# Optimization experiments

Measured on AMD Instinct MI355X. Metric: run time of the kernel, lower is better.

## Reference

```python
import jax, jax.numpy as jnp
import numpy as np

STRIDE = 1
PAD = 1
EXTENT = 3  # kernel footprint (ceil of max tap offset), 3x3 tap grid


def setup_inputs() -> dict:
    key = jax.random.key(0)
    k1, k2 = jax.random.split(key)
    B, Cin, H, W = 8, 64, 128, 128
    Cout, K = 64, 9
    x = jax.random.normal(k1, (B, Cin, H, W), dtype=jnp.float32)
    # per-tap weights, one scalar weight per (out_ch, in_ch, tap) -- op formula is 'x * w'
    weights = jax.random.normal(k2, (Cout, Cin, K), dtype=jnp.float32) * 0.05
    # 3x3 integer grid shifted by +0.4 -> non-integer offsets => bilinear (sub-pixel) gather
    base = jnp.stack(jnp.meshgrid(jnp.arange(3.0), jnp.arange(3.0), indexing='ij'), -1).reshape(9, 2)
    tap_offsets = (base + 0.4).astype(jnp.float32)  # [K, 2] (dy, dx)
    return {"x": x, "weights": weights, "tap_offsets": tap_offsets}


def _bilinear_tap(xp, dy, dx, H_out, W_out):
    # Gather xp at (oy*stride + dy, ox*stride + dx) with separable bilinear interp.
    Hp, Wp = xp.shape[-2], xp.shape[-1]
    y = jnp.arange(H_out, dtype=xp.dtype) * STRIDE + dy
    xc = jnp.arange(W_out, dtype=xp.dtype) * STRIDE + dx
    y0 = jnp.floor(y)
    x0 = jnp.floor(xc)
    fy = (y - y0)[None, None, :, None]
    fx = (xc - x0)[None, None, None, :]
    y0i = jnp.clip(y0.astype(jnp.int32), 0, Hp - 1)
    y1i = jnp.clip(y0.astype(jnp.int32) + 1, 0, Hp - 1)
    x0i = jnp.clip(x0.astype(jnp.int32), 0, Wp - 1)
    x1i = jnp.clip(x0.astype(jnp.int32) + 1, 0, Wp - 1)
    # interp rows first: [B, C, H_out, Wp]
    ry = xp[:, :, y0i, :] * (1.0 - fy) + xp[:, :, y1i, :] * fy
    # then columns: [B, C, H_out, W_out]
    return ry[:, :, :, x0i] * (1.0 - fx) + ry[:, :, :, x1i] * fx


def reference(x, weights, tap_offsets):
    B, Cin, H, W = x.shape
    K = weights.shape[-1]
    xp = jnp.pad(x, ((0, 0), (0, 0), (PAD, PAD), (PAD, PAD)))
    H_out = (H + 2 * PAD - EXTENT) // STRIDE + 1
    W_out = (W + 2 * PAD - EXTENT) // STRIDE + 1
    # gather all taps (loop over small fixed K=9, each fully vectorized over B,C,H,W)
    taps = [_bilinear_tap(xp, tap_offsets[k, 0], tap_offsets[k, 1], H_out, W_out)
            for k in range(K)]
    g = jnp.stack(taps, 0)  # [K, B, Cin, H_out, W_out]
    # per-tap op 'x * w', accumulated over taps and input channels
    return jnp.einsum('kbiyx,oik->boyx', g, weights)  # [B, Cout, H_out, W_out]
```

## Files before the change

### kernel.cpp

```cpp
#include <hip/hip_runtime.h>


#define CIN   64
#define COUT  64
#define HH    128
#define WW    128

typedef __attribute__((ext_vector_type(8)))  short bf16x8;
typedef __attribute__((ext_vector_type(4)))  float f32x4;
typedef __attribute__((ext_vector_type(16))) float f32x16;
typedef __attribute__((ext_vector_type(4)))  unsigned int u32x4;

__device__ __forceinline__ unsigned short f2bf(float f) {
  unsigned int u = __float_as_uint(f);
  u = (u + 0x7fffu + ((u >> 16) & 1u)) >> 16;
  return (unsigned short)u;
}

__global__ void make_wb(const float* __restrict__ wgt,
                        const float* __restrict__ off,
                        unsigned short* __restrict__ wb)
{
  int id = blockIdx.x * 64 + threadIdx.x;
  int o = id >> 6, c = id & 63;
  float W16[16];
  #pragma unroll
  for (int i = 0; i < 16; ++i) W16[i] = 0.f;
  for (int k = 0; k < 9; ++k) {
    float dy = off[2*k], dx = off[2*k+1];
    float fyf = floorf(dy), fxf = floorf(dx);
    int   iy = (int)fyf,   ix = (int)fxf;
    float fy = dy - fyf,   fx = dx - fxf;
    float wk = wgt[(o*CIN + c)*9 + k];
    W16[(iy  )*4 + ix  ] += wk * (1.f-fy)*(1.f-fx);
    W16[(iy  )*4 + ix+1] += wk * (1.f-fy)*fx;
    W16[(iy+1)*4 + ix  ] += wk * fy*(1.f-fx);
    W16[(iy+1)*4 + ix+1] += wk * fy*fx;
  }
  int g = c >> 4, half = (c >> 3) & 1, j = c & 7;
  int ni = o >> 5, l31 = o & 31;
  int lane = half*32 + l31;
  for (int tap = 0; tap < 16; ++tap) {
    int h8 = tap >> 3, rs8 = tap & 7;
    wb[(size_t)((((g*2 + h8)*16) + rs8*2 + ni)*64 + lane)*8 + j] = f2bf(W16[tap]);
  }
}

__global__ __launch_bounds__(128)
void transpose_x(const float* __restrict__ x, unsigned short* __restrict__ xt)
{
  const int bid = blockIdx.x;
  const int b   = bid / 131;
  const int yp  = bid - b * 131;
  const int t   = threadIdx.x;

  unsigned short* rowbase = xt + (size_t)(b*132 + yp)*8*132*8;

  if (yp == 0 || yp >= 129) {
    for (int i = t; i < 8*132; i += 128)
      *(u32x4*)&rowbase[i*8] = (u32x4){0u,0u,0u,0u};
    return;
  }
  const int gy = yp - 1;
  const int px = t;
  #pragma unroll
  for (int cq = 0; cq < 8; ++cq) {
    const float* ps = x + ((size_t)(b*CIN + cq*8)*HH + gy)*WW + px;
    float v[8];
    #pragma unroll
    for (int cc = 0; cc < 8; ++cc) v[cc] = ps[(size_t)cc*HH*WW];
    unsigned int pk[4];
    #pragma unroll
    for (int i = 0; i < 4; ++i)
      pk[i] = (unsigned int)f2bf(v[2*i]) | ((unsigned int)f2bf(v[2*i+1]) << 16);
    *(u32x4*)&rowbase[(cq*132 + px + 1)*8] = *(u32x4*)pk;
  }
  if (t < 32) {
    int cq = t >> 2, csel = t & 3;
    int col = (csel == 0) ? 0 : (128 + csel);
    *(u32x4*)&rowbase[(cq*132 + col)*8] = (u32x4){0u,0u,0u,0u};
  }
}

__global__ __launch_bounds__(256, 2)
void conv_mfma(const unsigned short* __restrict__ xt,
               const unsigned short* __restrict__ wb,
               float* __restrict__ out)
{
  const int wg = blockIdx.x;
  const int b  = wg & 7;
  const int i6 = wg >> 3;
  const int y0 = (i6 >> 1) * 4;
  const int x0 = (i6 & 1) * 64;
  const int t  = threadIdx.x;
  const int lane = t & 63;
  const int wave = t >> 6;
  const int l31  = lane & 31;
  const int half = lane >> 5;
  const int y    = y0 + wave;

  f32x16 acc[2][2];
  #pragma unroll
  for (int mi = 0; mi < 2; ++mi)
    #pragma unroll
    for (int ni = 0; ni < 2; ++ni)
      acc[mi][ni] = (f32x16)(0.f);

  const unsigned short* wl = wb + lane*8;

  const unsigned short* xbase = xt + (size_t)(b*132 + y)*8*132*8
                                   + (size_t)(x0 + l31)*8 + (size_t)half*132*8;

  bf16x8 aq[2][2], bq[2][2];

  auto loadB = [&](int g, int tap, bf16x8 (&dst)[2]) {
    int h8 = tap >> 3, rs8 = tap & 7;
    #pragma unroll
    for (int ni = 0; ni < 2; ++ni)
      dst[ni] = *(const bf16x8*)(wl + (size_t)(((g*2 + h8)*16) + rs8*2 + ni)*512);
  };
  auto loadA = [&](int g, int tap, bf16x8 (&dst)[2]) {
    int r = tap >> 2, s = tap & 3;
    const unsigned short* p = xbase + (size_t)(r*8*132 + g*2*132 + s)*8;
    #pragma unroll
    for (int mi = 0; mi < 2; ++mi)
      dst[mi] = *(const bf16x8*)(p + mi*32*8);
  };

  loadA(0, 0, aq[0]);
  loadB(0, 0, bq[0]);

  #pragma unroll
  for (int g = 0; g < 4; ++g) {
    #pragma unroll
    for (int tap = 0; tap < 16; ++tap) {
      if (tap < 15) {
        loadA(g, tap + 1, aq[(tap + 1) & 1]);
        loadB(g, tap + 1, bq[(tap + 1) & 1]);
      } else if (g < 3) {
        loadA(g + 1, 0, aq[0]);
        loadB(g + 1, 0, bq[0]);
      }
      const int sl = tap & 1;
      #pragma unroll
      for (int mi = 0; mi < 2; ++mi) {
        acc[mi][0] = __builtin_amdgcn_mfma_f32_32x32x16_bf16(aq[sl][mi], bq[sl][0], acc[mi][0], 0, 0, 0);
        acc[mi][1] = __builtin_amdgcn_mfma_f32_32x32x16_bf16(aq[sl][mi], bq[sl][1], acc[mi][1], 0, 0, 0);
      }
    }
  }

  #pragma unroll
  for (int mi = 0; mi < 2; ++mi) {
    #pragma unroll
    for (int ni = 0; ni < 2; ++ni) {
      int o = ni*32 + l31;
      float* dst = out + (((size_t)(b*COUT + o))*HH + y)*WW + x0 + mi*32 + 4*half;
      #pragma unroll
      for (int rg = 0; rg < 4; ++rg) {
        f32x4 v = (f32x4){acc[mi][ni][4*rg+0], acc[mi][ni][4*rg+1],
                          acc[mi][ni][4*rg+2], acc[mi][ni][4*rg+3]};
        *(f32x4*)(dst + 8*rg) = v;
      }
    }
  }
}

extern "C" void kernel_launch(void* const* d_in, const int* in_sizes, int n_in,
                              void* d_out, int out_size, void* d_ws, size_t ws_size,
                              hipStream_t stream)
{
  const float* x   = (const float*)d_in[0];
  const float* wgt = (const float*)d_in[1];
  const float* off = (const float*)d_in[2];
  float* out = (float*)d_out;

  unsigned short* wb = (unsigned short*)d_ws;
  unsigned short* xt = (unsigned short*)d_ws + 65536;

  make_wb<<<64, 64, 0, stream>>>(wgt, off, wb);
  transpose_x<<<8*131, 128, 0, stream>>>(x, xt);
  conv_mfma<<<512, 256, 0, stream>>>(xt, wb, out);
}
```

Baseline: 125.3 us.

## Stage input tile in LDS via global_load_lds and vectorize transpose

The conv kernel now copies a 7-row by 67-column input tile for all 64 channels into shared memory with direct global-to-LDS loads, then reads the A fragments from LDS. Previously each wave fetched overlapping tap windows from global memory, so neighbouring rows and shifted columns were loaded many times; staging the tile once removes that redundant global/L2 traffic. The weight fragments are now triple-buffered. The transpose kernel switches to 256 threads with float4 loads and a row pitch padded to 136, and its grid grows to cover 132 padded rows. The cost is about 64 KB of LDS per block, which limits occupancy to two blocks per CU, plus a block-wide barrier before any compute can start.

```diff
diff --git a/kernel.cpp b/kernel.cpp
--- a/kernel.cpp
+++ b/kernel.cpp
@@ -10,6 +10,9 @@
 typedef __attribute__((ext_vector_type(4)))  float f32x4;
 typedef __attribute__((ext_vector_type(16))) float f32x16;
 typedef __attribute__((ext_vector_type(4)))  unsigned int u32x4;
+
+#define AS1C(p) ((const __attribute__((address_space(1))) unsigned int*)(p))
+#define AS3P(p) ((__attribute__((address_space(3))) unsigned int*)(p))
 
 __device__ __forceinline__ unsigned short f2bf(float f) {
   unsigned int u = __float_as_uint(f);
@@ -46,47 +49,52 @@
   }
 }
 
-__global__ __launch_bounds__(128)
+__global__ __launch_bounds__(256)
 void transpose_x(const float* __restrict__ x, unsigned short* __restrict__ xt)
 {
   const int bid = blockIdx.x;
-  const int b   = bid / 131;
-  const int yp  = bid - b * 131;
+  const int b   = bid & 7;
+  const int yp  = bid >> 3;
   const int t   = threadIdx.x;
 
-  unsigned short* rowbase = xt + (size_t)(b*132 + yp)*8*132*8;
+  unsigned short* rowb = xt + (size_t)((b*132 + yp)*8)*136*8;
 
   if (yp == 0 || yp >= 129) {
-    for (int i = t; i < 8*132; i += 128)
-      *(u32x4*)&rowbase[i*8] = (u32x4){0u,0u,0u,0u};
+    for (int i = t; i < 8*136; i += 256)
+      *(u32x4*)&rowb[(size_t)i*8] = (u32x4){0u,0u,0u,0u};
     return;
   }
-  const int gy = yp - 1;
-  const int px = t;
+  const int gy  = yp - 1;
+  const int cq  = t >> 5;
+  const int seg = t & 31;
+  const f32x4* ps = (const f32x4*)(x + ((size_t)(b*CIN + cq*8)*HH + gy)*WW) + seg;
+  f32x4 v[8];
   #pragma unroll
-  for (int cq = 0; cq < 8; ++cq) {
-    const float* ps = x + ((size_t)(b*CIN + cq*8)*HH + gy)*WW + px;
-    float v[8];
-    #pragma unroll
-    for (int cc = 0; cc < 8; ++cc) v[cc] = ps[(size_t)cc*HH*WW];
+  for (int cc = 0; cc < 8; ++cc) v[cc] = ps[(size_t)cc*(HH*WW/4)];
+  #pragma unroll
+  for (int u = 0; u < 4; ++u) {
     unsigned int pk[4];
     #pragma unroll
     for (int i = 0; i < 4; ++i)
-      pk[i] = (unsigned int)f2bf(v[2*i]) | ((unsigned int)f2bf(v[2*i+1]) << 16);
-    *(u32x4*)&rowbase[(cq*132 + px + 1)*8] = *(u32x4*)pk;
+      pk[i] = (unsigned int)f2bf(v[2*i][u]) | ((unsigned int)f2bf(v[2*i+1][u]) << 16);
+    *(u32x4*)&rowb[(size_t)(cq*136 + seg*4 + u + 1)*8] = *(u32x4*)pk;
   }
-  if (t < 32) {
-    int cq = t >> 2, csel = t & 3;
-    int col = (csel == 0) ? 0 : (128 + csel);
-    *(u32x4*)&rowbase[(cq*132 + col)*8] = (u32x4){0u,0u,0u,0u};
+  if (t < 64) {
+    int c2 = t >> 3, ci = t & 7;
+    int col = ci ? (128 + ci) : 0;
+    *(u32x4*)&rowb[(size_t)(c2*136 + col)*8] = (u32x4){0u,0u,0u,0u};
   }
 }
+
+constexpr int LC = 72;
 
 __global__ __launch_bounds__(256, 2)
 void conv_mfma(const unsigned short* __restrict__ xt,
                const unsigned short* __restrict__ wb,
                float* __restrict__ out)
 {
+  __shared__ unsigned short lds[7*8*LC*8];
+
   const int wg = blockIdx.x;
   const int b  = wg & 7;
   const int i6 = wg >> 3;
@@ -99,6 +107,18 @@
   const int half = lane >> 5;
   const int y    = y0 + wave;
 
+  #pragma unroll
+  for (int i = 0; i < 14; ++i) {
+    int l   = wave*14 + i;
+    int row = l >> 3, cq = l & 7;
+    const unsigned short* gp = xt
+        + ((size_t)((b*132 + y0 + row)*8 + cq)*136 + x0)*8 + (size_t)lane*8;
+    unsigned short* lp = lds + (size_t)((row*8 + cq)*LC)*8;
+    __builtin_amdgcn_global_load_lds(AS1C(gp),      AS3P(lp),      16, 0, 0);
+    __builtin_amdgcn_global_load_lds(AS1C(gp + 32), AS3P(lp + 32), 16, 0, 0);
+  }
+  __syncthreads();
+
   f32x16 acc[2][2];
   #pragma unroll
   for (int mi = 0; mi < 2; ++mi)
@@ -107,46 +127,31 @@
       acc[mi][ni] = (f32x16)(0.f);
 
   const unsigned short* wl = wb + lane*8;
-
-  const unsigned short* xbase = xt + (size_t)(b*132 + y)*8*132*8
-                                   + (size_t)(x0 + l31)*8 + (size_t)half*132*8;
-
-  bf16x8 aq[2][2], bq[2][2];
-
-  auto loadB = [&](int g, int tap, bf16x8 (&dst)[2]) {
+  bf16x8 bq[3][2];
+  auto loadB = [&](int ki, bf16x8 (&d)[2]) {
+    int g = ki >> 4, tap = ki & 15;
     int h8 = tap >> 3, rs8 = tap & 7;
     #pragma unroll
     for (int ni = 0; ni < 2; ++ni)
-      dst[ni] = *(const bf16x8*)(wl + (size_t)(((g*2 + h8)*16) + rs8*2 + ni)*512);
+      d[ni] = *(const bf16x8*)(wl + (size_t)(((g*2 + h8)*16) + rs8*2 + ni)*512);
   };
-  auto loadA = [&](int g, int tap, bf16x8 (&dst)[2]) {
-    int r = tap >> 2, s = tap & 3;
-    const unsigned short* p = xbase + (size_t)(r*8*132 + g*2*132 + s)*8;
+  loadB(0, bq[0]);
+  loadB(1, bq[1]);
+
+  #pragma unroll
+  for (int ki = 0; ki < 64; ++ki) {
+    if (ki < 62) loadB(ki + 2, bq[(ki + 2) % 3]);
+    const int g = ki >> 4, tap = ki & 15;
+    const int r = tap >> 2, s = tap & 3;
+    bf16x8 afr[2];
     #pragma unroll
     for (int mi = 0; mi < 2; ++mi)
-      dst[mi] = *(const bf16x8*)(p + mi*32*8);
-  };
-
-  loadA(0, 0, aq[0]);
-  loadB(0, 0, bq[0]);
-
-  #pragma unroll
-  for (int g = 0; g < 4; ++g) {
+      afr[mi] = *(const bf16x8*)
+        &lds[(size_t)(((wave + r)*8 + g*2 + half)*LC + (mi*32 + l31 + s))*8];
     #pragma unroll
-    for (int tap = 0; tap < 16; ++tap) {
-      if (tap < 15) {
-        loadA(g, tap + 1, aq[(tap + 1) & 1]);
-        loadB(g, tap + 1, bq[(tap + 1) & 1]);
-      } else if (g < 3) {
-        loadA(g + 1, 0, aq[0]);
-        loadB(g + 1, 0, bq[0]);
-      }
-      const int sl = tap & 1;
-      #pragma unroll
-      for (int mi = 0; mi < 2; ++mi) {
-        acc[mi][0] = __builtin_amdgcn_mfma_f32_32x32x16_bf16(aq[sl][mi], bq[sl][0], acc[mi][0], 0, 0, 0);
-        acc[mi][1] = __builtin_amdgcn_mfma_f32_32x32x16_bf16(aq[sl][mi], bq[sl][1], acc[mi][1], 0, 0, 0);
-      }
+    for (int mi = 0; mi < 2; ++mi) {
+      acc[mi][0] = __builtin_amdgcn_mfma_f32_32x32x16_bf16(afr[mi], bq[ki % 3][0], acc[mi][0], 0, 0, 0);
+      acc[mi][1] = __builtin_amdgcn_mfma_f32_32x32x16_bf16(afr[mi], bq[ki % 3][1], acc[mi][1], 0, 0, 0);
     }
   }
 
@@ -179,6 +184,6 @@
   unsigned short* xt = (unsigned short*)d_ws + 65536;
 
   make_wb<<<64, 64, 0, stream>>>(wgt, off, wb);
-  transpose_x<<<8*131, 128, 0, stream>>>(x, xt);
+  transpose_x<<<1056, 256, 0, stream>>>(x, xt);
   conv_mfma<<<512, 256, 0, stream>>>(xt, wb, out);
 }
```

New measurement: 120.9 us. 3.6% less time.
